# Kernel optimization log

Hardware: AMD Instinct MI355X
Metric: run time of the kernel (lower is better)

Reference implementation:

```python
import jax, jax.numpy as jnp
import numpy as np

H = 4096          # hidden_size
I = 11008         # intermediate_size
G = 128           # AWQ group_size
# AWQ interleaved nibble order within each packed int32
_ORDER = jnp.array([0, 4, 1, 5, 2, 6, 3, 7], dtype=jnp.int32) * 4


def _mk_lin(key, K, N):
    k1, k2, k3 = jax.random.split(key, 3)
    qw = jax.random.randint(k1, (K, N // 8), 0, 100, dtype=jnp.int32)
    qz = jax.random.randint(k2, (K // G, N // 8), 0, 100, dtype=jnp.int32)
    sc = jax.random.normal(k3, (K // G, N), dtype=jnp.float32) * 0.02
    return qw, qz, sc


def setup_inputs() -> dict:
    key = jax.random.key(0)
    ks = jax.random.split(key, 7)
    x = jax.random.normal(ks[0], (8, 16, H), dtype=jnp.float32)
    ln1_w = jnp.ones((H,), dtype=jnp.float32)
    ln2_w = jnp.ones((H,), dtype=jnp.float32)
    qkv_qw, qkv_qz, qkv_sc = _mk_lin(ks[1], H, 3 * H)
    o_qw, o_qz, o_sc = _mk_lin(ks[2], H, H)
    gu_qw, gu_qz, gu_sc = _mk_lin(ks[3], H, 2 * I)
    dn_qw, dn_qz, dn_sc = _mk_lin(ks[4], I, H)
    return dict(x=x, ln1_w=ln1_w, ln2_w=ln2_w,
                qkv_qw=qkv_qw, qkv_qz=qkv_qz, qkv_sc=qkv_sc,
                o_qw=o_qw, o_qz=o_qz, o_sc=o_sc,
                gu_qw=gu_qw, gu_qz=gu_qz, gu_sc=gu_sc,
                dn_qw=dn_qw, dn_qz=dn_qz, dn_sc=dn_sc)


def rmsnorm(x, w, eps=1e-6):
    return x * jax.lax.rsqrt(jnp.mean(x * x, axis=-1, keepdims=True) + eps) * w


def dequant(qw, qz, sc):
    # qw: [K, N//8] int32 -> [K, N]; qz: [K//G, N//8] -> [K//G, N]
    K = qw.shape[0]
    N = sc.shape[1]
    w = ((qw[:, :, None] >> _ORDER) & 0xF).reshape(K, N).astype(sc.dtype)
    z = ((qz[:, :, None] >> _ORDER) & 0xF).reshape(K // G, N).astype(sc.dtype)
    return (w - jnp.repeat(z, G, axis=0)) * jnp.repeat(sc, G, axis=0)


def lite_linear(x, qw, qz, sc):
    return x @ dequant(qw, qz, sc)


def reference(x, ln1_w, ln2_w,
              qkv_qw, qkv_qz, qkv_sc,
              o_qw, o_qz, o_sc,
              gu_qw, gu_qz, gu_sc,
              dn_qw, dn_qz, dn_sc):
    residual = x
    h = rmsnorm(x, ln1_w)
    h = lite_linear(h, qkv_qw, qkv_qz, qkv_sc)[..., :H]  # mock attn: take q slice
    h = lite_linear(h, o_qw, o_qz, o_sc)
    h = residual + h
    residual = h
    h = rmsnorm(h, ln2_w)
    gate_up = lite_linear(h, gu_qw, gu_qz, gu_sc)
    gate, up = gate_up[..., :I], gate_up[..., I:]
    h = lite_linear(jax.nn.silu(gate) * up, dn_qw, dn_qz, dn_sc)
    return residual + h
```

## Files before the change

kernel.cpp:

```cpp
#include <hip/hip_runtime.h>

typedef unsigned int   u32;
typedef unsigned short u16;

typedef _Float16 h2  __attribute__((ext_vector_type(2)));
typedef _Float16 h8  __attribute__((ext_vector_type(8)));
typedef float    f32x4 __attribute__((ext_vector_type(4)));

#define M_TOK 128

__device__ __forceinline__ u16 f2h_(float f) {
    _Float16 h = (_Float16)f; return __builtin_bit_cast(u16, h);
}
__device__ __forceinline__ float h2f_(u16 b) {
    _Float16 h = __builtin_bit_cast(_Float16, b); return (float)h;
}
__device__ __forceinline__ void acc8(uint4 v, float* s) {
#pragma unroll
    for (int i = 0; i < 4; ++i) {
        u32 w = ((const u32*)&v)[i];
        s[2 * i]     += h2f_((u16)(w & 0xFFFF));
        s[2 * i + 1] += h2f_((u16)(w >> 16));
    }
}

__constant__ int SHC[8] = {0, 16, 4, 20, 8, 24, 12, 28};

__launch_bounds__(256)
__global__ void pack_zs(const int* __restrict__ qz, const float* __restrict__ sc,
                        u32* __restrict__ zs, int qws, int scs, int Ncols, int total) {
    const int idx = blockIdx.x * 256 + threadIdx.x;
    if (idx >= total) return;
    const int g = idx / Ncols, n = idx - g * Ncols;
    const u32 d = (u32)qz[(size_t)g * qws + (n >> 3)];
    const u32 zj = (d >> SHC[n & 7]) & 15u;
    const u32 mz = 0xE400u | zj;
    const u16 sh = f2h_(sc[(size_t)g * scs + n]);
    zs[(size_t)g * Ncols + n] = mz | ((u32)sh << 16);
}


__launch_bounds__(256)
__global__ void rmsnorm_k(const float* __restrict__ in, const float* __restrict__ w,
                          u16* __restrict__ out) {
    const int row = blockIdx.x;
    const float* x = in + (size_t)row * 4096;
    float ss = 0.f;
#pragma unroll
    for (int j = 0; j < 16; ++j) {
        float v = x[threadIdx.x + 256 * j];
        ss += v * v;
    }
#pragma unroll
    for (int off = 32; off > 0; off >>= 1) ss += __shfl_down(ss, off, 64);
    __shared__ float ws4[4];
    if ((threadIdx.x & 63) == 0) ws4[threadIdx.x >> 6] = ss;
    __syncthreads();
    float total = ws4[0] + ws4[1] + ws4[2] + ws4[3];
    float r = rsqrtf(total * (1.f / 4096.f) + 1e-6f);
    const int mt = row >> 4, l16 = row & 15;
#pragma unroll
    for (int c2 = 0; c2 < 2; ++c2) {
        int c = threadIdx.x * 2 + c2;
        int kb = c >> 2, qq = c & 3;
        u16 o8[8];
#pragma unroll
        for (int j = 0; j < 8; ++j) {
            int i = c * 8 + j;
            o8[j] = f2h_(x[i] * r * w[i]);
        }
        *(uint4*)(out + ((size_t)(kb * 8 + mt) * 64 + qq * 16 + l16) * 8) = *(const uint4*)o8;
    }
}

__launch_bounds__(256, 4)
__global__ void gemm_awq(const u16* __restrict__ A, const u32* __restrict__ zs,
                         const int* __restrict__ qw, u16* __restrict__ part,
                         int qws, int N, int K, int kchunk) {
    __shared__ __align__(16) char ldsB[4 * 2304];

    const int tid = threadIdx.x, w = tid >> 6, lane = tid & 63;
    const int q = lane >> 4, l16 = lane & 15;
    const int n0w = blockIdx.x * 64 + w * 16;
    const int pc0 = n0w >> 3;
    const int kp = lane & 31, h = lane >> 5;
    const int sk = blockIdx.y, kc0 = sk * kchunk, kend = min(kc0 + kchunk, K);

    char* myB   = ldsB + w * 2304;
    char* wbase = myB + kp * 4;
    const u16* Ala = A + lane * 8;
    const int* qws_base = qw + pc0;
    const u32* zsO = zs + n0w + h * 8;

    f32x4 acc[8] = {};
    uint4 za0, za1;

    auto ldraw = [&](int k0) -> uint2 {
        return *(const uint2*)(qws_base + (size_t)(k0 + lane) * qws);
    };
    auto loadzs = [&](int g) {
        za0 = *(const uint4*)(zsO + (size_t)g * N);
        za1 = *(const uint4*)(zsO + (size_t)g * N + 4);
    };
    auto route = [&](uint2 rv, u32& w0, u32& w1) {
        const int i0 = kp * 8, i1 = i0 + 4;
        int b00 = __builtin_amdgcn_ds_bpermute(i0, (int)rv.x);
        int b01 = __builtin_amdgcn_ds_bpermute(i1, (int)rv.x);
        int b10 = __builtin_amdgcn_ds_bpermute(i0, (int)rv.y);
        int b11 = __builtin_amdgcn_ds_bpermute(i1, (int)rv.y);
        w0 = (u32)(h ? b10 : b00);
        w1 = (u32)(h ? b11 : b01);
    };
    auto emit8 = [&](u32 w0, u32 w1, uint4 z0, uint4 z1) {
        char* bb = wbase + (h * 8) * 144;
        u32 w0s = w0 >> 4, w1s = w1 >> 4;
        auto em = [&](int j, u32 a0, u32 a1, int b, u32 zsj) {
            h2 mz = __builtin_bit_cast(h2, __builtin_amdgcn_perm(zsj, zsj, 0x01000100u));
            h2 s2 = __builtin_bit_cast(h2, __builtin_amdgcn_perm(zsj, zsj, 0x03020302u));
            u32 t = __builtin_amdgcn_perm(a1, a0, (u32)(b | ((b + 4) << 16)));
            u32 u = (t & 0x000F000Fu) | 0x64006400u;
            h2 v = (__builtin_bit_cast(h2, u) + mz) * s2;
            *(u32*)(bb + j * 144) = __builtin_bit_cast(u32, v);
        };
        em(0, w0, w1, 0, z0.x);  em(4, w0, w1, 1, z1.x);
        em(1, w0, w1, 2, z0.y);  em(5, w0, w1, 3, z1.y);
        em(2, w0s, w1s, 0, z0.z); em(6, w0s, w1s, 1, z1.z);
        em(3, w0s, w1s, 2, z0.w); em(7, w0s, w1s, 3, z1.w);
    };

    uint2 rv_n = {0, 0};

    loadzs(kc0 >> 7);
    uint2 rv0 = ldraw(kc0);
    if (kc0 + 64 < kend) rv_n = ldraw(kc0 + 64);
    {
        u32 w0, w1;
        route(rv0, w0, w1);
        emit8(w0, w1, za0, za1);
    }
    if (((kc0 + 64) & 127) == 0 && kc0 + 64 < kend)
        loadzs((kc0 + 64) >> 7);

    for (int k0 = kc0; k0 < kend; k0 += 64) {
        const bool kn1 = (k0 + 64) < kend, kn2 = (k0 + 128) < kend;
        const int kb0 = k0 >> 5;
        uint4 bv0 = *(const uint4*)(myB + l16 * 144 + q * 16);
        uint4 bv1 = *(const uint4*)(myB + l16 * 144 + 64 + q * 16);
        uint4 af0[8];
#pragma unroll
        for (int mt = 0; mt < 8; ++mt)
            af0[mt] = *(const uint4*)(Ala + (size_t)(kb0 * 8 + mt) * 512);
        uint2 rv_f = {0, 0};
        if (kn2) rv_f = ldraw(k0 + 128);
        if (kn1) {
            u32 w0, w1;
            route(rv_n, w0, w1);
            emit8(w0, w1, za0, za1);
        }
        if (kn2 && (((k0 + 128) & 127) == 0))
            loadzs((k0 + 128) >> 7);
#pragma unroll
        for (int mt = 0; mt < 8; ++mt)
            acc[mt] = __builtin_amdgcn_mfma_f32_16x16x32_f16(
                __builtin_bit_cast(h8, af0[mt]), __builtin_bit_cast(h8, bv0),
                acc[mt], 0, 0, 0);
        uint4 af1[8];
#pragma unroll
        for (int mt = 0; mt < 8; ++mt)
            af1[mt] = *(const uint4*)(Ala + (size_t)((kb0 + 1) * 8 + mt) * 512);
#pragma unroll
        for (int mt = 0; mt < 8; ++mt)
            acc[mt] = __builtin_amdgcn_mfma_f32_16x16x32_f16(
                __builtin_bit_cast(h8, af1[mt]), __builtin_bit_cast(h8, bv1),
                acc[mt], 0, 0, 0);
        rv_n = rv_f;
    }

    u16* pp = part + (size_t)sk * M_TOK * N;
    const int n = n0w + l16;
#pragma unroll
    for (int mt = 0; mt < 8; ++mt)
#pragma unroll
        for (int r = 0; r < 4; ++r) {
            const int m = mt * 16 + q * 4 + r;
            pp[(size_t)m * N + n] = f2h_(acc[mt][r]);
        }
}

__launch_bounds__(256)
__global__ void reduce_to_afrag(const u16* __restrict__ part, u16* __restrict__ out,
                                int SK) {
    const int idx = blockIdx.x * 256 + threadIdx.x;
    const int m = idx >> 9, c = idx & 511;
    float s[8] = {};
    for (int k = 0; k < SK; ++k)
        acc8(*(const uint4*)(part + (size_t)k * 524288 + (size_t)m * 4096 + c * 8), s);
    const int kb = c >> 2, qq = c & 3, mt = m >> 4, l16 = m & 15;
    u16 o8[8];
#pragma unroll
    for (int j = 0; j < 8; ++j) o8[j] = f2h_(s[j]);
    *(uint4*)(out + ((size_t)(kb * 8 + mt) * 64 + qq * 16 + l16) * 8) = *(const uint4*)o8;
}

__launch_bounds__(256)
__global__ void reduce_add_f32(const u16* __restrict__ part, const float* __restrict__ resin,
                               float* __restrict__ out, int SK) {
    const int idx = blockIdx.x * 256 + threadIdx.x;
    const size_t base = (size_t)idx * 8;
    float s[8];
    *(float4*)&s[0] = *(const float4*)(resin + base);
    *(float4*)&s[4] = *(const float4*)(resin + base + 4);
    for (int k = 0; k < SK; ++k)
        acc8(*(const uint4*)(part + (size_t)k * 524288 + base), s);
    *(float4*)(out + base)     = *(const float4*)&s[0];
    *(float4*)(out + base + 4) = *(const float4*)&s[4];
}

__launch_bounds__(256)
__global__ void silu_mul(const u16* __restrict__ part, u16* __restrict__ act) {
    const int idx = blockIdx.x * 256 + threadIdx.x;
    const int m = idx / 1376, c = idx - m * 1376;
    const int nb = c * 8;
    float g[8] = {}, u[8] = {};
    for (int k = 0; k < 3; ++k) {
        const size_t base = (size_t)k * 2818048 + (size_t)m * 22016 + nb;
        acc8(*(const uint4*)(part + base), g);
        acc8(*(const uint4*)(part + base + 11008), u);
    }
    const int kb = nb >> 5, qq = (nb >> 3) & 3, mt = m >> 4, l16 = m & 15;
    u16 o8[8];
#pragma unroll
    for (int j = 0; j < 8; ++j) {
        float a = g[j] / (1.f + __expf(-g[j])) * u[j];
        o8[j] = f2h_(a);
    }
    *(uint4*)(act + ((size_t)(kb * 8 + mt) * 64 + qq * 16 + l16) * 8) = *(const uint4*)o8;
}

extern "C" void kernel_launch(void* const* d_in, const int* in_sizes, int n_in,
                              void* d_out, int out_size, void* d_ws, size_t ws_size,
                              hipStream_t stream) {
    const float* x      = (const float*)d_in[0];
    const float* ln1_w  = (const float*)d_in[1];
    const float* ln2_w  = (const float*)d_in[2];
    const int*   qkv_qw = (const int*)d_in[3];
    const int*   qkv_qz = (const int*)d_in[4];
    const float* qkv_sc = (const float*)d_in[5];
    const int*   o_qw   = (const int*)d_in[6];
    const int*   o_qz   = (const int*)d_in[7];
    const float* o_sc   = (const float*)d_in[8];
    const int*   gu_qw  = (const int*)d_in[9];
    const int*   gu_qz  = (const int*)d_in[10];
    const float* gu_sc  = (const float*)d_in[11];
    const int*   dn_qw  = (const int*)d_in[12];
    const int*   dn_qz  = (const int*)d_in[13];
    const float* dn_sc  = (const float*)d_in[14];
    float* out = (float*)d_out;

    char* ws = (char*)d_ws;
    u16*   pbuf = (u16*)(ws);
    u32*   zsb  = (u32*)(ws + 16908288);
    u16*   act  = (u16*)(ws + 19726336);
    float* res2 = (float*)(ws + 22544384);
    u16*   slot = (u16*)(ws + 24641536);

    rmsnorm_k<<<128, 256, 0, stream>>>(x, ln1_w, slot);
    pack_zs<<<512, 256, 0, stream>>>(qkv_qz, qkv_sc, zsb, 1536, 12288, 4096, 131072);

    gemm_awq<<<dim3(64, 16), 256, 0, stream>>>(slot, zsb, qkv_qw, pbuf,
                                               1536, 4096, 4096, 256);
    reduce_to_afrag<<<256, 256, 0, stream>>>(pbuf, slot, 16);
    pack_zs<<<512, 256, 0, stream>>>(o_qz, o_sc, zsb, 512, 4096, 4096, 131072);

    gemm_awq<<<dim3(64, 16), 256, 0, stream>>>(slot, zsb, o_qw, pbuf,
                                               512, 4096, 4096, 256);
    reduce_add_f32<<<256, 256, 0, stream>>>(pbuf, x, res2, 16);

    rmsnorm_k<<<128, 256, 0, stream>>>(res2, ln2_w, slot);
    pack_zs<<<2752, 256, 0, stream>>>(gu_qz, gu_sc, zsb, 2752, 22016, 22016, 704512);

    gemm_awq<<<dim3(344, 3), 256, 0, stream>>>(slot, zsb, gu_qw, pbuf,
                                               2752, 22016, 4096, 1408);
    silu_mul<<<688, 256, 0, stream>>>(pbuf, act);
    pack_zs<<<1376, 256, 0, stream>>>(dn_qz, dn_sc, zsb, 512, 4096, 4096, 352256);

    gemm_awq<<<dim3(64, 16), 256, 0, stream>>>(act, zsb, dn_qw, pbuf,
                                               512, 4096, 11008, 704);
    reduce_add_f32<<<256, 256, 0, stream>>>(pbuf, res2, out, 16);
}
```

Baseline: 343.6 us.

## Transpose packed AWQ weights and use register-dequant 64x64 MFMA GEMM tiles

Adds a pack_qwt kernel that transposes each packed int4 weight matrix so K is contiguous per column group. A new gemm8 kernel dequantises in registers straight into MFMA B fragments, dropping the LDS staging and ds_bpermute routing. Each wave computes a 64x64 tile, with the M dimension split across blockIdx.z. The gate/up projection becomes two GEMMs with a reduce_gate plus silu8 reduction. The cost is an extra full weight transpose pass over global memory every call, plus more kernel launches.

```diff
diff --git a/kernel.cpp b/kernel.cpp
--- a/kernel.cpp
+++ b/kernel.cpp
@@ -6,6 +6,7 @@
 typedef _Float16 h2  __attribute__((ext_vector_type(2)));
 typedef _Float16 h8  __attribute__((ext_vector_type(8)));
 typedef float    f32x4 __attribute__((ext_vector_type(4)));
+typedef u32      u32x4 __attribute__((ext_vector_type(4)));
 
 #define M_TOK 128
 
@@ -39,6 +40,24 @@
     zs[(size_t)g * Ncols + n] = mz | ((u32)sh << 16);
 }
 
+__launch_bounds__(256)
+__global__ void pack_qwt(const int* __restrict__ qw, u32* __restrict__ qwt,
+                         int qws, int col0, int K) {
+    __shared__ u32 tile[16 * 64];
+    const int t = threadIdx.x;
+    const int k0 = blockIdx.x * 64, c0 = blockIdx.y * 16;
+    const int r = t >> 2, cq = (t & 3) * 4;
+    uint4 v = *(const uint4*)(qw + (size_t)(k0 + r) * qws + col0 + c0 + cq);
+    tile[(cq + 0) * 64 + r] = v.x;
+    tile[(cq + 1) * 64 + r] = v.y;
+    tile[(cq + 2) * 64 + r] = v.z;
+    tile[(cq + 3) * 64 + r] = v.w;
+    __syncthreads();
+    const int cl = t >> 4, kl = (t & 15) * 4;
+    uint4 o = *(const uint4*)&tile[cl * 64 + kl];
+    *(uint4*)(qwt + (size_t)(c0 + cl) * K + k0 + kl) = o;
+}
+
 
 __launch_bounds__(256)
 __global__ void rmsnorm_k(const float* __restrict__ in, const float* __restrict__ w,
@@ -73,117 +92,113 @@
     }
 }
 
-__launch_bounds__(256, 4)
-__global__ void gemm_awq(const u16* __restrict__ A, const u32* __restrict__ zs,
-                         const int* __restrict__ qw, u16* __restrict__ part,
-                         int qws, int N, int K, int kchunk) {
-    __shared__ __align__(16) char ldsB[4 * 2304];
-
+struct Raw { uint4 a, b; };
+
+__launch_bounds__(256, 2)
+__global__ void gemm8(const u16* __restrict__ A, const u32* __restrict__ zs,
+                      const u32* __restrict__ qwt, u16* __restrict__ part,
+                      int K, int kchunk, int Nz, int Np) {
     const int tid = threadIdx.x, w = tid >> 6, lane = tid & 63;
     const int q = lane >> 4, l16 = lane & 15;
-    const int n0w = blockIdx.x * 64 + w * 16;
-    const int pc0 = n0w >> 3;
-    const int kp = lane & 31, h = lane >> 5;
+    const int n0w = blockIdx.x * 256 + w * 64;
+    const int mh  = blockIdx.z;
     const int sk = blockIdx.y, kc0 = sk * kchunk, kend = min(kc0 + kchunk, K);
-
-    char* myB   = ldsB + w * 2304;
-    char* wbase = myB + kp * 4;
-    const u16* Ala = A + lane * 8;
-    const int* qws_base = qw + pc0;
-    const u32* zsO = zs + n0w + h * 8;
-
-    f32x4 acc[8] = {};
-    uint4 za0, za1;
-
-    auto ldraw = [&](int k0) -> uint2 {
-        return *(const uint2*)(qws_base + (size_t)(k0 + lane) * qws);
-    };
-    auto loadzs = [&](int g) {
-        za0 = *(const uint4*)(zsO + (size_t)g * N);
-        za1 = *(const uint4*)(zsO + (size_t)g * N + 4);
-    };
-    auto route = [&](uint2 rv, u32& w0, u32& w1) {
-        const int i0 = kp * 8, i1 = i0 + 4;
-        int b00 = __builtin_amdgcn_ds_bpermute(i0, (int)rv.x);
-        int b01 = __builtin_amdgcn_ds_bpermute(i1, (int)rv.x);
-        int b10 = __builtin_amdgcn_ds_bpermute(i0, (int)rv.y);
-        int b11 = __builtin_amdgcn_ds_bpermute(i1, (int)rv.y);
-        w0 = (u32)(h ? b10 : b00);
-        w1 = (u32)(h ? b11 : b01);
-    };
-    auto emit8 = [&](u32 w0, u32 w1, uint4 z0, uint4 z1) {
-        char* bb = wbase + (h * 8) * 144;
-        u32 w0s = w0 >> 4, w1s = w1 >> 4;
-        auto em = [&](int j, u32 a0, u32 a1, int b, u32 zsj) {
-            h2 mz = __builtin_bit_cast(h2, __builtin_amdgcn_perm(zsj, zsj, 0x01000100u));
-            h2 s2 = __builtin_bit_cast(h2, __builtin_amdgcn_perm(zsj, zsj, 0x03020302u));
-            u32 t = __builtin_amdgcn_perm(a1, a0, (u32)(b | ((b + 4) << 16)));
-            u32 u = (t & 0x000F000Fu) | 0x64006400u;
-            h2 v = (__builtin_bit_cast(h2, u) + mz) * s2;
-            *(u32*)(bb + j * 144) = __builtin_bit_cast(u32, v);
+    const int j = l16 & 7;
+    const u32 sh = (u32)(((j & 1) << 4) | ((j >> 1) << 2));
+
+    const u32* qp[4];
+#pragma unroll
+    for (int nt = 0; nt < 4; ++nt)
+        qp[nt] = qwt + (size_t)((n0w + nt * 16 + l16) >> 3) * K + q * 8;
+    const u32* zsl = zs + n0w + l16;
+    const u16* Ala = A + lane * 8 + (size_t)mh * 4 * 512;
+
+    f32x4 acc[4][4] = {};
+    h2 mzv[4], s2v[4];
+    u32 zq[4];
+
+    auto ldz = [&](int g) {
+#pragma unroll
+        for (int nt = 0; nt < 4; ++nt) zq[nt] = zsl[(size_t)g * Nz + nt * 16];
+    };
+    auto cvtz = [&]() {
+#pragma unroll
+        for (int nt = 0; nt < 4; ++nt) {
+            mzv[nt] = __builtin_bit_cast(h2, __builtin_amdgcn_perm(zq[nt], zq[nt], 0x01000100u));
+            s2v[nt] = __builtin_bit_cast(h2, __builtin_amdgcn_perm(zq[nt], zq[nt], 0x03020302u));
+        }
+    };
+    auto ldraw = [&](int k, Raw* r) {
+#pragma unroll
+        for (int nt = 0; nt < 4; ++nt) {
+            r[nt].a = *(const uint4*)(qp[nt] + k);
+            r[nt].b = *(const uint4*)(qp[nt] + k + 4);
+        }
+    };
+    auto lda = [&](int k, uint4* a) {
+        const int kb = k >> 5;
+#pragma unroll
+        for (int mt = 0; mt < 4; ++mt)
+            a[mt] = *(const uint4*)(Ala + (size_t)(kb * 8 + mt) * 512);
+    };
+    auto deq = [&](const Raw& r, int nt) -> h8 {
+        u32 t0 = r.a.x >> sh, t1 = r.a.y >> sh, t2 = r.a.z >> sh, t3 = r.a.w >> sh;
+        u32 t4 = r.b.x >> sh, t5 = r.b.y >> sh, t6 = r.b.z >> sh, t7 = r.b.w >> sh;
+        u32x4 o;
+        auto em = [&](u32 te, u32 to) -> u32 {
+            u32 u = (__builtin_amdgcn_perm(to, te, 0x00040000u) & 0x000F000Fu) | 0x64006400u;
+            h2 v = (__builtin_bit_cast(h2, u) + mzv[nt]) * s2v[nt];
+            return __builtin_bit_cast(u32, v);
         };
-        em(0, w0, w1, 0, z0.x);  em(4, w0, w1, 1, z1.x);
-        em(1, w0, w1, 2, z0.y);  em(5, w0, w1, 3, z1.y);
-        em(2, w0s, w1s, 0, z0.z); em(6, w0s, w1s, 1, z1.z);
-        em(3, w0s, w1s, 2, z0.w); em(7, w0s, w1s, 3, z1.w);
-    };
-
-    uint2 rv_n = {0, 0};
-
-    loadzs(kc0 >> 7);
-    uint2 rv0 = ldraw(kc0);
-    if (kc0 + 64 < kend) rv_n = ldraw(kc0 + 64);
-    {
-        u32 w0, w1;
-        route(rv0, w0, w1);
-        emit8(w0, w1, za0, za1);
-    }
-    if (((kc0 + 64) & 127) == 0 && kc0 + 64 < kend)
-        loadzs((kc0 + 64) >> 7);
-
-    for (int k0 = kc0; k0 < kend; k0 += 64) {
-        const bool kn1 = (k0 + 64) < kend, kn2 = (k0 + 128) < kend;
-        const int kb0 = k0 >> 5;
-        uint4 bv0 = *(const uint4*)(myB + l16 * 144 + q * 16);
-        uint4 bv1 = *(const uint4*)(myB + l16 * 144 + 64 + q * 16);
-        uint4 af0[8];
-#pragma unroll
-        for (int mt = 0; mt < 8; ++mt)
-            af0[mt] = *(const uint4*)(Ala + (size_t)(kb0 * 8 + mt) * 512);
-        uint2 rv_f = {0, 0};
-        if (kn2) rv_f = ldraw(k0 + 128);
-        if (kn1) {
-            u32 w0, w1;
-            route(rv_n, w0, w1);
-            emit8(w0, w1, za0, za1);
-        }
-        if (kn2 && (((k0 + 128) & 127) == 0))
-            loadzs((k0 + 128) >> 7);
-#pragma unroll
-        for (int mt = 0; mt < 8; ++mt)
-            acc[mt] = __builtin_amdgcn_mfma_f32_16x16x32_f16(
-                __builtin_bit_cast(h8, af0[mt]), __builtin_bit_cast(h8, bv0),
-                acc[mt], 0, 0, 0);
-        uint4 af1[8];
-#pragma unroll
-        for (int mt = 0; mt < 8; ++mt)
-            af1[mt] = *(const uint4*)(Ala + (size_t)((kb0 + 1) * 8 + mt) * 512);
-#pragma unroll
-        for (int mt = 0; mt < 8; ++mt)
-            acc[mt] = __builtin_amdgcn_mfma_f32_16x16x32_f16(
-                __builtin_bit_cast(h8, af1[mt]), __builtin_bit_cast(h8, bv1),
-                acc[mt], 0, 0, 0);
-        rv_n = rv_f;
-    }
-
-    u16* pp = part + (size_t)sk * M_TOK * N;
-    const int n = n0w + l16;
-#pragma unroll
-    for (int mt = 0; mt < 8; ++mt)
-#pragma unroll
-        for (int r = 0; r < 4; ++r) {
-            const int m = mt * 16 + q * 4 + r;
-            pp[(size_t)m * N + n] = f2h_(acc[mt][r]);
+        o.x = em(t0, t1); o.y = em(t2, t3); o.z = em(t4, t5); o.w = em(t6, t7);
+        return __builtin_bit_cast(h8, o);
+    };
+
+    Raw rA[4], rB[4];
+    uint4 av[4];
+
+    ldz(kc0 >> 7);
+    ldraw(kc0, rA);
+    if (kc0 + 32 < kend) ldraw(kc0 + 32, rB);
+    cvtz();
+
+    auto body = [&](int k0, Raw* rcur) {
+        const bool kn1 = (k0 + 32) < kend, kn2 = (k0 + 64) < kend;
+        lda(k0, av);
+        if (kn2 && (((k0 + 64) & 127) == 0)) ldz((k0 + 64) >> 7);
+#pragma unroll
+        for (int nt = 0; nt < 4; ++nt) {
+            h8 b = deq(rcur[nt], nt);
+            if (kn2) {
+                rcur[nt].a = *(const uint4*)(qp[nt] + k0 + 64);
+                rcur[nt].b = *(const uint4*)(qp[nt] + k0 + 68);
+            }
+#pragma unroll
+            for (int mt = 0; mt < 4; ++mt)
+                acc[mt][nt] = __builtin_amdgcn_mfma_f32_16x16x32_f16(
+                    __builtin_bit_cast(h8, av[mt]), b, acc[mt][nt], 0, 0, 0);
+        }
+        if (kn1 && (((k0 + 32) & 127) == 0)) cvtz();
+    };
+
+    for (int k0 = kc0;;) {
+        body(k0, rA);
+        k0 += 32; if (k0 >= kend) break;
+        body(k0, rB);
+        k0 += 32; if (k0 >= kend) break;
+    }
+
+    u16* pp = part + (size_t)sk * M_TOK * Np;
+#pragma unroll
+    for (int mt = 0; mt < 4; ++mt)
+#pragma unroll
+        for (int nt = 0; nt < 4; ++nt) {
+            const int n = n0w + nt * 16 + l16;
+#pragma unroll
+            for (int r = 0; r < 4; ++r) {
+                const int m = mh * 64 + mt * 16 + q * 4 + r;
+                pp[(size_t)m * Np + n] = f2h_(acc[mt][nt][r]);
+            }
         }
 }
 
@@ -217,16 +232,29 @@
 }
 
 __launch_bounds__(256)
-__global__ void silu_mul(const u16* __restrict__ part, u16* __restrict__ act) {
+__global__ void reduce_gate(const u16* __restrict__ part, u16* __restrict__ gate16) {
+    const int idx = blockIdx.x * 256 + threadIdx.x;
+    const size_t base = (size_t)idx * 8;
+    float s[8] = {};
+    for (int k = 0; k < 6; ++k)
+        acc8(*(const uint4*)(part + (size_t)k * 1409024 + base), s);
+    u16 o8[8];
+#pragma unroll
+    for (int j = 0; j < 8; ++j) o8[j] = f2h_(s[j]);
+    *(uint4*)(gate16 + base) = *(const uint4*)o8;
+}
+
+__launch_bounds__(256)
+__global__ void silu8(const u16* __restrict__ part, const u16* __restrict__ gate16,
+                      u16* __restrict__ act) {
     const int idx = blockIdx.x * 256 + threadIdx.x;
     const int m = idx / 1376, c = idx - m * 1376;
     const int nb = c * 8;
+    const size_t base = (size_t)m * 11008 + nb;
     float g[8] = {}, u[8] = {};
-    for (int k = 0; k < 3; ++k) {
-        const size_t base = (size_t)k * 2818048 + (size_t)m * 22016 + nb;
-        acc8(*(const uint4*)(part + base), g);
-        acc8(*(const uint4*)(part + base + 11008), u);
-    }
+    acc8(*(const uint4*)(gate16 + base), g);
+    for (int k = 0; k < 6; ++k)
+        acc8(*(const uint4*)(part + (size_t)k * 1409024 + base), u);
     const int kb = nb >> 5, qq = (nb >> 3) & 3, mt = m >> 4, l16 = m & 15;
     u16 o8[8];
 #pragma unroll
@@ -258,33 +286,39 @@
     float* out = (float*)d_out;
 
     char* ws = (char*)d_ws;
-    u16*   pbuf = (u16*)(ws);
-    u32*   zsb  = (u32*)(ws + 16908288);
-    u16*   act  = (u16*)(ws + 19726336);
-    float* res2 = (float*)(ws + 22544384);
-    u16*   slot = (u16*)(ws + 24641536);
+    u16*   pbuf   = (u16*)(ws);
+    u32*   qwt    = (u32*)(ws + 16908288);
+    u32*   zsb    = (u32*)(ws + 39452672);
+    u16*   gate16 = (u16*)(ws + 42270720);
+    u16*   act    = (u16*)(ws + 45088768);
+    float* res2   = (float*)(ws + 47906816);
+    u16*   slot   = (u16*)(ws + 50003968);
 
     rmsnorm_k<<<128, 256, 0, stream>>>(x, ln1_w, slot);
+
     pack_zs<<<512, 256, 0, stream>>>(qkv_qz, qkv_sc, zsb, 1536, 12288, 4096, 131072);
-
-    gemm_awq<<<dim3(64, 16), 256, 0, stream>>>(slot, zsb, qkv_qw, pbuf,
-                                               1536, 4096, 4096, 256);
+    pack_qwt<<<dim3(64, 32), 256, 0, stream>>>(qkv_qw, qwt, 1536, 0, 4096);
+    gemm8<<<dim3(16, 16, 2), 256, 0, stream>>>(slot, zsb, qwt, pbuf, 4096, 256, 4096, 4096);
     reduce_to_afrag<<<256, 256, 0, stream>>>(pbuf, slot, 16);
+
     pack_zs<<<512, 256, 0, stream>>>(o_qz, o_sc, zsb, 512, 4096, 4096, 131072);
-
-    gemm_awq<<<dim3(64, 16), 256, 0, stream>>>(slot, zsb, o_qw, pbuf,
-                                               512, 4096, 4096, 256);
+    pack_qwt<<<dim3(64, 32), 256, 0, stream>>>(o_qw, qwt, 512, 0, 4096);
+    gemm8<<<dim3(16, 16, 2), 256, 0, stream>>>(slot, zsb, qwt, pbuf, 4096, 256, 4096, 4096);
     reduce_add_f32<<<256, 256, 0, stream>>>(pbuf, x, res2, 16);
 
     rmsnorm_k<<<128, 256, 0, stream>>>(res2, ln2_w, slot);
+
     pack_zs<<<2752, 256, 0, stream>>>(gu_qz, gu_sc, zsb, 2752, 22016, 22016, 704512);
-
-    gemm_awq<<<dim3(344, 3), 256, 0, stream>>>(slot, zsb, gu_qw, pbuf,
-                                               2752, 22016, 4096, 1408);
-    silu_mul<<<688, 256, 0, stream>>>(pbuf, act);
+    pack_qwt<<<dim3(64, 86), 256, 0, stream>>>(gu_qw, qwt, 2752, 0, 4096);
+    gemm8<<<dim3(43, 6, 2), 256, 0, stream>>>(slot, zsb, qwt, pbuf, 4096, 704, 22016, 11008);
+    reduce_gate<<<688, 256, 0, stream>>>(pbuf, gate16);
+
+    pack_qwt<<<dim3(64, 86), 256, 0, stream>>>(gu_qw, qwt, 2752, 1376, 4096);
+    gemm8<<<dim3(43, 6, 2), 256, 0, stream>>>(slot, zsb + 11008, qwt, pbuf, 4096, 704, 22016, 11008);
+    silu8<<<688, 256, 0, stream>>>(pbuf, gate16, act);
+
     pack_zs<<<1376, 256, 0, stream>>>(dn_qz, dn_sc, zsb, 512, 4096, 4096, 352256);
-
-    gemm_awq<<<dim3(64, 16), 256, 0, stream>>>(act, zsb, dn_qw, pbuf,
-                                               512, 4096, 11008, 704);
+    pack_qwt<<<dim3(172, 32), 256, 0, stream>>>(dn_qw, qwt, 512, 0, 11008);
+    gemm8<<<dim3(16, 16, 2), 256, 0, stream>>>(act, zsb, qwt, pbuf, 11008, 704, 4096, 4096);
     reduce_add_f32<<<256, 256, 0, stream>>>(pbuf, res2, out, 16);
 }
```

Result: slower. 385.8 us (+12.3%).
